# Kernel tuning notes

Measured on AMD Instinct MI355X. Metric: run time of the kernel, lower is better.

The kernel has to match this reference:

```python
import jax, jax.numpy as jnp
import numpy as np

E, H, W = 1024, 16, 256  # embed_dim, num_heads, window_size
D = E // H               # head_dim


def _rmsnorm(t, w):
    eps = jnp.finfo(t.dtype).eps
    return t * jax.lax.rsqrt(jnp.mean(t * t, axis=-1, keepdims=True) + eps) * w


def setup_inputs() -> dict:
    key = jax.random.key(0)
    ks = jax.random.split(key, 11)
    B, T = 2, 2048
    s = 1.0 / np.sqrt(E)
    return {
        "x": jax.random.normal(ks[0], (B, T, E), jnp.float32),
        "wq": jax.random.normal(ks[1], (E, E), jnp.float32) * s,
        "bq": jnp.zeros((E,), jnp.float32),
        "wk": jax.random.normal(ks[2], (E, E), jnp.float32) * s,
        "bk": jnp.zeros((E,), jnp.float32),
        "wv": jax.random.normal(ks[3], (E, E), jnp.float32) * s,
        "bv": jnp.zeros((E,), jnp.float32),
        "wo": jax.random.normal(ks[4], (E, E), jnp.float32) * s,
        "bo": jnp.zeros((E,), jnp.float32),
        "qn_w": jnp.ones((D,), jnp.float32),
        "kn_w": jnp.ones((D,), jnp.float32),
    }


def reference(x, wq, bq, wk, bk, wv, bv, wo, bo, qn_w, kn_w):
    B, T, _ = x.shape
    # projections; weights stored (in, out)
    q = (x @ wq + bq).reshape(B, T, H, D).transpose(0, 2, 1, 3)  # [B,H,T,D]
    k = (x @ wk + bk).reshape(B, T, H, D).transpose(0, 2, 1, 3)
    v = (x @ wv + bv).reshape(B, T, H, D).transpose(0, 2, 1, 3)
    q = _rmsnorm(q, qn_w)
    k = _rmsnorm(k, kn_w)

    scores = jnp.einsum("bhqd,bhkd->bhqk", q, k) / jnp.sqrt(jnp.float32(D))
    row = jnp.arange(T)[:, None]
    col = jnp.arange(T)[None, :]
    invalid = (col > row) | (row - col >= W)  # causal + sliding window
    neg_inf = jnp.float32(-jnp.inf)
    scores = jnp.where(invalid, neg_inf, scores)

    # genetic fitness reweighting
    masked_attn = jnp.where(invalid, 0.0, jax.nn.softmax(scores, axis=-1))
    gene_means = jnp.mean(jax.nn.sigmoid(masked_attn), axis=-1)  # [B,H,T]
    denom = gene_means + 0.5
    sum_inv = jnp.sum(1.0 / denom, axis=2, keepdims=True)        # [B,H,1]
    fitness = 1.0 / (denom * sum_inv)                            # [B,H,T]
    scores = scores + jnp.log(fitness)[..., None]

    attn = jax.nn.softmax(scores, axis=-1)
    out = jnp.einsum("bhqk,bhkd->bhqd", attn, v)
    out = out.transpose(0, 2, 1, 3).reshape(B, T, E)
    return out @ wo + bo
```

## Files before the change

kernel.cpp:

```cpp
#include <hip/hip_runtime.h>

typedef _Float16 f16;
typedef _Float16 f16x4 __attribute__((ext_vector_type(4)));
typedef _Float16 f16x8 __attribute__((ext_vector_type(8)));
typedef float f32x4 __attribute__((ext_vector_type(4)));

#define MFMA16(a, b, c) __builtin_amdgcn_mfma_f32_16x16x32_f16(a, b, c, 0, 0, 0)

constexpr int T = 2048;
constexpr int E = 1024;
constexpr int H = 16;
constexpr int D = 64;
constexpr int WIN = 256;
#define NEGF (-1e30f)
#define L2E 1.4426950408889634f

__device__ __forceinline__ void gload16(const f16* g, f16* l) {
  __builtin_amdgcn_global_load_lds(
      (__attribute__((address_space(1))) void*)(void*)g,
      (__attribute__((address_space(3))) void*)(void*)l, 16, 0, 0);
}

__global__ __launch_bounds__(256) void cast_x_kernel(const float* __restrict__ x,
                                                     f16* __restrict__ xb) {
  int idx = (blockIdx.x * 256 + threadIdx.x) * 4;
  float4 v = *(const float4*)(x + idx);
  f16x4 o = {(f16)v.x, (f16)v.y, (f16)v.z, (f16)v.w};
  *(f16x4*)(xb + idx) = o;
}

__global__ __launch_bounds__(256) void transpose_w_kernel(
    const float* __restrict__ w0, const float* __restrict__ w1,
    const float* __restrict__ w2, const float* __restrict__ w3,
    f16* __restrict__ o0, f16* __restrict__ o1, f16* __restrict__ o2,
    f16* __restrict__ o3) {
  int z = blockIdx.z;
  const float* w = z == 0 ? w0 : z == 1 ? w1 : z == 2 ? w2 : w3;
  f16* o = z == 0 ? o0 : z == 1 ? o1 : z == 2 ? o2 : o3;
  __shared__ float tile[64][65];
  int k0 = blockIdx.x * 64, n0 = blockIdx.y * 64;
  int r = threadIdx.x >> 2, cb = (threadIdx.x & 3) * 16;
  const float* src = w + (size_t)(k0 + r) * E + n0 + cb;
#pragma unroll
  for (int j = 0; j < 16; j += 4) {
    float4 v = *(const float4*)(src + j);
    tile[r][cb + j] = v.x;
    tile[r][cb + j + 1] = v.y;
    tile[r][cb + j + 2] = v.z;
    tile[r][cb + j + 3] = v.w;
  }
  __syncthreads();
  f16 tmp[16];
#pragma unroll
  for (int j = 0; j < 16; ++j) tmp[j] = (f16)tile[cb + j][r];
  f16* dst = o + (size_t)(n0 + r) * E + k0 + cb;
  *(f16x8*)dst = *(f16x8*)&tmp[0];
  *(f16x8*)(dst + 8) = *(f16x8*)&tmp[8];
}

template <int QKV>
__global__ __launch_bounds__(256) void gemm_bt_kernel(
    const f16* __restrict__ A, const f16* __restrict__ B0,
    const f16* __restrict__ B1, const f16* __restrict__ B2,
    const float* __restrict__ c0, const float* __restrict__ c1,
    const float* __restrict__ c2, const float* __restrict__ qnw,
    const float* __restrict__ knw, f16* __restrict__ oq, f16* __restrict__ ok,
    f16* __restrict__ Vt, float* __restrict__ of32, int M, int N, int K) {
  int z = blockIdx.z;
  const f16* Bt = z == 0 ? B0 : z == 1 ? B1 : B2;
  const float* bias = z == 0 ? c0 : z == 1 ? c1 : c2;

  __shared__ f16 lA[8192];
  __shared__ f16 lB[8192];

  int m0 = blockIdx.x * 128, n0 = blockIdx.y * 128;
  int tid = threadIdx.x;
  int wid = tid >> 6, lane = tid & 63;
  int wm = wid >> 1, wn = wid & 1;
  int lr = lane & 15, lg = lane >> 4;

  f32x4 zero = {0.f, 0.f, 0.f, 0.f};
  f32x4 acc[4][4];
  for (int a = 0; a < 4; ++a)
    for (int b = 0; b < 4; ++b) acc[a][b] = zero;

  int srow = (lane >> 3);
  int scol = ((lane & 7) << 3);

  for (int k0 = 0; k0 < K; k0 += 64) {
    __syncthreads();
#pragma unroll
    for (int p = 0; p < 4; ++p) {
      int cc = (wid << 2) + p;
      int row = (cc << 3) + srow;
      int gc = scol ^ ((row & 7) << 3);
      gload16(A + (size_t)(m0 + row) * K + k0 + gc, &lA[cc << 9]);
      gload16(Bt + (size_t)(n0 + row) * K + k0 + gc, &lB[cc << 9]);
    }
    __syncthreads();
#pragma unroll
    for (int kk = 0; kk < 2; ++kk) {
      int kc = kk * 32 + (lg << 3);
      f16x8 af[4], bf[4];
#pragma unroll
      for (int mt = 0; mt < 4; ++mt) {
        int row = wm * 64 + mt * 16 + lr;
        af[mt] = *(const f16x8*)&lA[((row << 6) + kc) ^ ((row & 7) << 3)];
      }
#pragma unroll
      for (int nt = 0; nt < 4; ++nt) {
        int row = wn * 64 + nt * 16 + lr;
        bf[nt] = *(const f16x8*)&lB[((row << 6) + kc) ^ ((row & 7) << 3)];
      }
#pragma unroll
      for (int mt = 0; mt < 4; ++mt)
#pragma unroll
        for (int nt = 0; nt < 4; ++nt)
          acc[mt][nt] = MFMA16(af[mt], bf[nt], acc[mt][nt]);
    }
  }

  if constexpr (QKV == 1) {
    if (z < 2) {
      const float* nw = z == 0 ? qnw : knw;
      f16* o = z == 0 ? oq : ok;
      const float eps = 1.1920929e-7f;
      float wv_[4];
#pragma unroll
      for (int nt = 0; nt < 4; ++nt) wv_[nt] = nw[nt * 16 + lr];
#pragma unroll
      for (int mt = 0; mt < 4; ++mt) {
        float vbuf[4][4];
        float ss[4] = {0.f, 0.f, 0.f, 0.f};
#pragma unroll
        for (int nt = 0; nt < 4; ++nt) {
          float bv = bias[n0 + wn * 64 + nt * 16 + lr];
#pragma unroll
          for (int i = 0; i < 4; ++i) {
            float v = acc[mt][nt][i] + bv;
            vbuf[nt][i] = v;
            ss[i] += v * v;
          }
        }
        float rr[4];
#pragma unroll
        for (int i = 0; i < 4; ++i) {
          ss[i] += __shfl_xor(ss[i], 1);
          ss[i] += __shfl_xor(ss[i], 2);
          ss[i] += __shfl_xor(ss[i], 4);
          ss[i] += __shfl_xor(ss[i], 8);
          rr[i] = rsqrtf(ss[i] * (1.0f / 64.0f) + eps);
        }
        int row = m0 + wm * 64 + mt * 16 + (lg << 2);
#pragma unroll
        for (int nt = 0; nt < 4; ++nt) {
          int col = n0 + wn * 64 + nt * 16 + lr;
#pragma unroll
          for (int i = 0; i < 4; ++i)
            o[(size_t)(row + i) * N + col] = (f16)(vbuf[nt][i] * rr[i] * wv_[nt]);
        }
      }
    } else {
#pragma unroll
      for (int mt = 0; mt < 4; ++mt) {
        int row = m0 + wm * 64 + mt * 16 + (lg << 2);
        int b = row >> 11;
        int t = row & (T - 1);
#pragma unroll
        for (int nt = 0; nt < 4; ++nt) {
          int col = n0 + wn * 64 + nt * 16 + lr;
          float bv = bias[col];
          int h = col >> 6, d = col & 63;
          f16x4 pk = {(f16)(acc[mt][nt][0] + bv), (f16)(acc[mt][nt][1] + bv),
                      (f16)(acc[mt][nt][2] + bv), (f16)(acc[mt][nt][3] + bv)};
          *(f16x4*)&Vt[(((size_t)(b * H + h) * D + d) << 11) + t] = pk;
        }
      }
    }
  } else {
#pragma unroll
    for (int mt = 0; mt < 4; ++mt) {
#pragma unroll
      for (int nt = 0; nt < 4; ++nt) {
        int row = m0 + wm * 64 + mt * 16 + (lg << 2);
        int col = n0 + wn * 64 + nt * 16 + lr;
        float bv = bias[col];
#pragma unroll
        for (int i = 0; i < 4; ++i)
          of32[(size_t)(row + i) * N + col] = acc[mt][nt][i] + bv;
      }
    }
  }
}

__global__ __launch_bounds__(256) void attn_kernel(const f16* __restrict__ qn,
                                                   const f16* __restrict__ kn,
                                                   const f16* __restrict__ Vt,
                                                   f16* __restrict__ aout) {
  int q0 = blockIdx.x * 64;
  int bh = blockIdx.y;
  int b = bh >> 4, h = bh & 15;
  int tid = threadIdx.x;
  int w = tid >> 6, lane = tid & 63;
  int lr = lane & 15, lg = lane >> 4;

  __shared__ f16 lK[4096];
  __shared__ f16 lV[4096];
  __shared__ f16 lP[4096];

  const f16* Qb = qn + (size_t)(b * T + q0 + w * 16 + lr) * E + h * 64 + (lg << 3);
  f16x8 qf0 = *(const f16x8*)Qb;
  f16x8 qf1 = *(const f16x8*)(Qb + 32);

  f32x4 zero = {0.f, 0.f, 0.f, 0.f};
  f32x4 acc[4] = {zero, zero, zero, zero};
  float m[4] = {NEGF, NEGF, NEGF, NEGF};
  float l[4] = {0.f, 0.f, 0.f, 0.f};

  int mi = q0 >> 6;
  int kts = mi - 4 < 0 ? 0 : mi - 4;

  const f16* Kbase = kn + (size_t)b * T * E + h * 64;
  const f16* Vbase = Vt + (size_t)bh * D * T;

  for (int kt = kts; kt <= mi; ++kt) {
    int k0 = kt * 64;
    __syncthreads();
#pragma unroll
    for (int p = 0; p < 2; ++p) {
      int e = (tid + p * 256) * 8;
      int row = e >> 6, col = e & 63;
      f16x8 kv = *(const f16x8*)(Kbase + (size_t)(k0 + row) * E + col);
      f16x8 vv = *(const f16x8*)(Vbase + (size_t)row * T + k0 + col);
      int se = e ^ ((row & 7) << 3);
      *(f16x8*)&lK[se] = kv;
      *(f16x8*)&lV[se] = vv;
    }
    __syncthreads();

    f32x4 s[4];
#pragma unroll
    for (int ct = 0; ct < 4; ++ct) s[ct] = zero;
#pragma unroll
    for (int kk = 0; kk < 2; ++kk) {
      int kc = kk * 32 + (lg << 3);
#pragma unroll
      for (int ct = 0; ct < 4; ++ct) {
        int row = ct * 16 + lr;
        f16x8 bf = *(const f16x8*)&lK[((row << 6) + kc) ^ ((row & 7) << 3)];
        s[ct] = MFMA16(kk == 0 ? qf0 : qf1, bf, s[ct]);
      }
    }

    float tm[4] = {NEGF, NEGF, NEGF, NEGF};
    int rowg0 = q0 + w * 16 + (lg << 2);
#pragma unroll
    for (int ct = 0; ct < 4; ++ct) {
      int col = k0 + ct * 16 + lr;
#pragma unroll
      for (int i = 0; i < 4; ++i) {
        int rowg = rowg0 + i;
        float v = s[ct][i] * 0.125f;
        if (col > rowg || rowg - col >= WIN) v = NEGF;
        s[ct][i] = v;
        tm[i] = fmaxf(tm[i], v);
      }
    }
#pragma unroll
    for (int i = 0; i < 4; ++i) {
      tm[i] = fmaxf(tm[i], __shfl_xor(tm[i], 1));
      tm[i] = fmaxf(tm[i], __shfl_xor(tm[i], 2));
      tm[i] = fmaxf(tm[i], __shfl_xor(tm[i], 4));
      tm[i] = fmaxf(tm[i], __shfl_xor(tm[i], 8));
    }
    float fac[4], ps[4];
#pragma unroll
    for (int i = 0; i < 4; ++i) {
      float mn = fmaxf(m[i], tm[i]);
      fac[i] = exp2f((m[i] - mn) * L2E);
      m[i] = mn;
      ps[i] = 0.f;
    }
#pragma unroll
    for (int ct = 0; ct < 4; ++ct)
#pragma unroll
      for (int i = 0; i < 4; ++i) {
        float p = exp2f((s[ct][i] - m[i]) * L2E);
        s[ct][i] = p;
        ps[i] += p;
      }
#pragma unroll
    for (int i = 0; i < 4; ++i) {
      ps[i] += __shfl_xor(ps[i], 1);
      ps[i] += __shfl_xor(ps[i], 2);
      ps[i] += __shfl_xor(ps[i], 4);
      ps[i] += __shfl_xor(ps[i], 8);
      l[i] = l[i] * fac[i] + ps[i];
    }
#pragma unroll
    for (int dt = 0; dt < 4; ++dt)
#pragma unroll
      for (int i = 0; i < 4; ++i) acc[dt][i] *= fac[i];

#pragma unroll
    for (int ct = 0; ct < 4; ++ct)
#pragma unroll
      for (int i = 0; i < 4; ++i) {
        int qloc = (lg << 2) + i;
        int el = (qloc << 6) + ct * 16 + lr;
        lP[w * 1024 + (el ^ ((qloc & 7) << 3))] = (f16)s[ct][i];
      }

#pragma unroll
    for (int kk = 0; kk < 2; ++kk) {
      int kc = kk * 32 + (lg << 3);
      int ep = w * 1024 + (((lr << 6) + kc) ^ ((lr & 7) << 3));
      f16x8 pf = *(const f16x8*)&lP[ep];
#pragma unroll
      for (int dt = 0; dt < 4; ++dt) {
        int row = dt * 16 + lr;
        f16x8 vf = *(const f16x8*)&lV[((row << 6) + kc) ^ ((row & 7) << 3)];
        acc[dt] = MFMA16(pf, vf, acc[dt]);
      }
    }
  }

#pragma unroll
  for (int i = 0; i < 4; ++i) {
    float inv = 1.0f / l[i];
    int tok = q0 + w * 16 + (lg << 2) + i;
    f16* dst = aout + (size_t)(b * T + tok) * E + h * 64 + lr;
#pragma unroll
    for (int dt = 0; dt < 4; ++dt) dst[dt * 16] = (f16)(acc[dt][i] * inv);
  }
}

extern "C" void kernel_launch(void* const* d_in, const int* in_sizes, int n_in,
                              void* d_out, int out_size, void* d_ws,
                              size_t ws_size, hipStream_t stream) {
  const float* x = (const float*)d_in[0];
  const float* wq = (const float*)d_in[1];
  const float* bq = (const float*)d_in[2];
  const float* wk = (const float*)d_in[3];
  const float* bk = (const float*)d_in[4];
  const float* wv = (const float*)d_in[5];
  const float* bv = (const float*)d_in[6];
  const float* wo = (const float*)d_in[7];
  const float* bo = (const float*)d_in[8];
  const float* qn_w = (const float*)d_in[9];
  const float* kn_w = (const float*)d_in[10];
  float* out = (float*)d_out;

  char* ws = (char*)d_ws;
  const size_t MB = 1u << 20;
  f16* xb = (f16*)(ws);
  f16* wqT = (f16*)(ws + 8 * MB);
  f16* wkT = (f16*)(ws + 10 * MB);
  f16* wvT = (f16*)(ws + 12 * MB);
  f16* woT = (f16*)(ws + 14 * MB);
  f16* qn = (f16*)(ws + 16 * MB);
  f16* kn = (f16*)(ws + 24 * MB);
  f16* Vt = (f16*)(ws + 32 * MB);
  f16* aout = (f16*)(ws + 40 * MB);

  cast_x_kernel<<<4096, 256, 0, stream>>>(x, xb);
  transpose_w_kernel<<<dim3(16, 16, 4), 256, 0, stream>>>(wq, wk, wv, wo, wqT,
                                                          wkT, wvT, woT);
  gemm_bt_kernel<1><<<dim3(32, 8, 3), 256, 0, stream>>>(
      xb, wqT, wkT, wvT, bq, bk, bv, qn_w, kn_w, qn, kn, Vt, nullptr, 4096,
      1024, 1024);
  attn_kernel<<<dim3(32, 32), 256, 0, stream>>>(qn, kn, Vt, aout);
  gemm_bt_kernel<0><<<dim3(32, 8, 1), 256, 0, stream>>>(
      aout, woT, woT, woT, bo, bo, bo, nullptr, nullptr, nullptr, nullptr,
      nullptr, out, 4096, 1024, 1024);
}
```

Measured before the change: 113.0 us.

## Double-buffer LDS tiles in GEMM and attention kernels to overlap loads

```diff
diff --git a/kernel.cpp b/kernel.cpp
--- a/kernel.cpp
+++ b/kernel.cpp
@@ -70,8 +70,8 @@
   const f16* Bt = z == 0 ? B0 : z == 1 ? B1 : B2;
   const float* bias = z == 0 ? c0 : z == 1 ? c1 : c2;
 
-  __shared__ f16 lA[8192];
-  __shared__ f16 lB[8192];
+  __shared__ f16 lA[2][8192];
+  __shared__ f16 lB[2][8192];
 
   int m0 = blockIdx.x * 128, n0 = blockIdx.y * 128;
   int tid = threadIdx.x;
@@ -84,20 +84,26 @@
   for (int a = 0; a < 4; ++a)
     for (int b = 0; b < 4; ++b) acc[a][b] = zero;
 
-  int srow = (lane >> 3);
-  int scol = ((lane & 7) << 3);
-
-  for (int k0 = 0; k0 < K; k0 += 64) {
-    __syncthreads();
+  int srow = lane >> 3;
+  int scol = (lane & 7) << 3;
+
+  auto stage = [&](int buf, int k0) {
 #pragma unroll
     for (int p = 0; p < 4; ++p) {
       int cc = (wid << 2) + p;
       int row = (cc << 3) + srow;
       int gc = scol ^ ((row & 7) << 3);
-      gload16(A + (size_t)(m0 + row) * K + k0 + gc, &lA[cc << 9]);
-      gload16(Bt + (size_t)(n0 + row) * K + k0 + gc, &lB[cc << 9]);
-    }
-    __syncthreads();
+      gload16(A + (size_t)(m0 + row) * K + k0 + gc, &lA[buf][cc << 9]);
+      gload16(Bt + (size_t)(n0 + row) * K + k0 + gc, &lB[buf][cc << 9]);
+    }
+  };
+
+  int nit = K >> 6;
+  stage(0, 0);
+  __syncthreads();
+  int cur = 0;
+  for (int t = 0; t < nit; ++t) {
+    if (t + 1 < nit) stage(cur ^ 1, (t + 1) << 6);
 #pragma unroll
     for (int kk = 0; kk < 2; ++kk) {
       int kc = kk * 32 + (lg << 3);
@@ -105,18 +111,22 @@
 #pragma unroll
       for (int mt = 0; mt < 4; ++mt) {
         int row = wm * 64 + mt * 16 + lr;
-        af[mt] = *(const f16x8*)&lA[((row << 6) + kc) ^ ((row & 7) << 3)];
+        af[mt] = *(const f16x8*)&lA[cur][((row << 6) + kc) ^ ((row & 7) << 3)];
       }
 #pragma unroll
       for (int nt = 0; nt < 4; ++nt) {
         int row = wn * 64 + nt * 16 + lr;
-        bf[nt] = *(const f16x8*)&lB[((row << 6) + kc) ^ ((row & 7) << 3)];
+        bf[nt] = *(const f16x8*)&lB[cur][((row << 6) + kc) ^ ((row & 7) << 3)];
       }
 #pragma unroll
       for (int mt = 0; mt < 4; ++mt)
 #pragma unroll
         for (int nt = 0; nt < 4; ++nt)
           acc[mt][nt] = MFMA16(af[mt], bf[nt], acc[mt][nt]);
+    }
+    if (t + 1 < nit) {
+      __syncthreads();
+      cur ^= 1;
     }
   }
 
@@ -204,8 +214,8 @@
   int w = tid >> 6, lane = tid & 63;
   int lr = lane & 15, lg = lane >> 4;
 
-  __shared__ f16 lK[4096];
-  __shared__ f16 lV[4096];
+  __shared__ f16 lK[2][4096];
+  __shared__ f16 lV[2][4096];
   __shared__ f16 lP[4096];
 
   const f16* Qb = qn + (size_t)(b * T + q0 + w * 16 + lr) * E + h * 64 + (lg << 3);
@@ -223,20 +233,28 @@
   const f16* Kbase = kn + (size_t)b * T * E + h * 64;
   const f16* Vbase = Vt + (size_t)bh * D * T;
 
+  int srow = lane >> 3;
+  int scol = (lane & 7) << 3;
+
+  auto stageKV = [&](int buf, int kt) {
+    int k0 = kt << 6;
+#pragma unroll
+    for (int p = 0; p < 2; ++p) {
+      int cc = (w << 1) + p;
+      int row = (cc << 3) + srow;
+      int gc = scol ^ ((row & 7) << 3);
+      gload16(Kbase + (size_t)(k0 + row) * E + gc, &lK[buf][cc << 9]);
+      gload16(Vbase + (size_t)row * T + k0 + gc, &lV[buf][cc << 9]);
+    }
+  };
+
+  stageKV(0, kts);
+  __syncthreads();
+  int cur = 0;
+
   for (int kt = kts; kt <= mi; ++kt) {
-    int k0 = kt * 64;
-    __syncthreads();
-#pragma unroll
-    for (int p = 0; p < 2; ++p) {
-      int e = (tid + p * 256) * 8;
-      int row = e >> 6, col = e & 63;
-      f16x8 kv = *(const f16x8*)(Kbase + (size_t)(k0 + row) * E + col);
-      f16x8 vv = *(const f16x8*)(Vbase + (size_t)row * T + k0 + col);
-      int se = e ^ ((row & 7) << 3);
-      *(f16x8*)&lK[se] = kv;
-      *(f16x8*)&lV[se] = vv;
-    }
-    __syncthreads();
+    if (kt < mi) stageKV(cur ^ 1, kt + 1);
+    int k0 = kt << 6;
 
     f32x4 s[4];
 #pragma unroll
@@ -247,7 +265,7 @@
 #pragma unroll
       for (int ct = 0; ct < 4; ++ct) {
         int row = ct * 16 + lr;
-        f16x8 bf = *(const f16x8*)&lK[((row << 6) + kc) ^ ((row & 7) << 3)];
+        f16x8 bf = *(const f16x8*)&lK[cur][((row << 6) + kc) ^ ((row & 7) << 3)];
         s[ct] = MFMA16(kk == 0 ? qf0 : qf1, bf, s[ct]);
       }
     }
@@ -319,9 +337,14 @@
 #pragma unroll
       for (int dt = 0; dt < 4; ++dt) {
         int row = dt * 16 + lr;
-        f16x8 vf = *(const f16x8*)&lV[((row << 6) + kc) ^ ((row & 7) << 3)];
+        f16x8 vf = *(const f16x8*)&lV[cur][((row << 6) + kc) ^ ((row & 7) << 3)];
         acc[dt] = MFMA16(pf, vf, acc[dt]);
       }
+    }
+
+    if (kt < mi) {
+      __syncthreads();
+      cur ^= 1;
     }
   }
 
```

Measured after the change: 106.6 us. 5.7% less time.
